# Optimization experiments

Hardware: AMD Instinct MI355X
Metric: run time of the kernel (lower is better)

Reference implementation:

```python
import jax, jax.numpy as jnp
import numpy as np

N_CHANNELS = 270
N_SUBJECTS = 200
B, T = 256, 1024


def setup_inputs() -> dict:
    key = jax.random.key(0)
    k_x, k_s = jax.random.split(key)
    x = jax.random.normal(k_x, (B, N_CHANNELS, T), dtype=jnp.float32)
    subjects = jax.random.randint(k_s, (B,), 0, N_SUBJECTS, dtype=jnp.int64)
    # init_id=True: weights start as identity, then divided by sqrt(C)
    weights = jnp.broadcast_to(jnp.eye(N_CHANNELS, dtype=jnp.float32),
                               (N_SUBJECTS, N_CHANNELS, N_CHANNELS)) / np.sqrt(N_CHANNELS)
    return {"x": x, "subjects": subjects, "weights": weights}


def reference(x, subjects, weights):
    # Gather per-sample CxC weight, then batched matmul: bct,bcd->bdt
    w = weights[subjects]  # (B, C, C)
    return jnp.einsum('bct,bcd->bdt', x, w)
```

## Files before the change

kernel.cpp:

```cpp
#include <hip/hip_runtime.h>


#define C_    270
#define T_    1024
#define B_    256
#define NSUB_ 200

#define BM 64
#define BN 128
#define BK 32
#define NK 9
#define ROWU32 20
#define BOFF (BM * ROWU32)
#define LDSU32 ((BM + BN) * ROWU32)

typedef __attribute__((ext_vector_type(8))) short bf16x8;
typedef __attribute__((ext_vector_type(4))) float f32x4;
typedef __attribute__((ext_vector_type(2))) float f32x2;
typedef __attribute__((ext_vector_type(2))) unsigned u32x2;
typedef __attribute__((ext_vector_type(4))) int i32x4;

__device__ __forceinline__ unsigned pk(float lo, float hi) {
    unsigned r;
    asm("v_cvt_pk_bf16_f32 %0, %1, %2" : "=v"(r) : "v"(lo), "v"(hi));
    return r;
}

__device__ __forceinline__ void tile_barrier() {
    asm volatile("s_waitcnt lgkmcnt(0)" ::: "memory");
    __builtin_amdgcn_s_barrier();
}

template<bool SW>
__device__ __forceinline__ bf16x8 ldfrag(const unsigned* p) {
    i32x4 u = *(const i32x4*)p;
    if (SW) { i32x4 v = {u[2], u[3], u[0], u[1]}; return __builtin_bit_cast(bf16x8, v); }
    return __builtin_bit_cast(bf16x8, u);
}

__global__ __launch_bounds__(256, 3)
void subj_layers_kernel(const float* __restrict__ x,
                        const int* __restrict__ subjects,
                        const float* __restrict__ w,
                        float* __restrict__ out)
{
    __shared__ unsigned lds[2][LDSU32];

    const int tid  = threadIdx.x;
    const int lane = tid & 63;
    const int wid  = tid >> 6;
    const int wr   = wid >> 1;
    const int wc   = wid & 1;
    const int lg   = lane >> 4;
    const int lr   = lane & 15;

    const int bid  = (blockIdx.x & 7) * 1280 + (blockIdx.x >> 3);
    const int b    = bid / 40;
    const int rem  = bid % 40;
    const int d0   = (rem % 5) * BM;
    const int t0   = (rem / 5) * BN;

    int sub = subjects[b];
    sub = sub < 0 ? 0 : (sub >= NSUB_ ? NSUB_ - 1 : sub);
    const float* __restrict__ wsub = w + (size_t)sub * (C_ * C_);
    const float* __restrict__ xb   = x + (size_t)b * (C_ * T_);

    const int btq = tid & 31;
    const int bcq = tid >> 5;
    const float* __restrict__ xbt = xb + (t0 + 4 * btq);
    const int colB = 2 * (bcq ^ ((btq >> 2) & 7));
    const int adp = tid & 31;
    const int acq = tid >> 5;
    const int dA  = d0 + 2 * adp;
    const bool dAok = (dA + 1 < C_);
    const int colA = 2 * (acq ^ ((adp >> 3) & 7));

    f32x4 acc[2][4];
    #pragma unroll
    for (int m = 0; m < 2; ++m)
        #pragma unroll
        for (int n = 0; n < 4; ++n)
            acc[m][n] = (f32x4){0.f, 0.f, 0.f, 0.f};

    f32x4 pb[4];
    f32x2 pa[4];

    auto load_tiles = [&](int c0, bool full) {
        #pragma unroll
        for (int e = 0; e < 4; ++e) {
            const int c = c0 + 4 * bcq + e;
            pb[e] = (full || c < C_) ? *(const f32x4*)(xbt + (size_t)c * T_)
                                     : (f32x4){0.f, 0.f, 0.f, 0.f};
        }
        #pragma unroll
        for (int e = 0; e < 4; ++e) {
            const int c = c0 + 4 * acq + e;
            pa[e] = (dAok && (full || c < C_)) ? *(const f32x2*)(wsub + (size_t)c * C_ + dA)
                                               : (f32x2){0.f, 0.f};
        }
    };

    auto store_tiles = [&](unsigned* L) {
        unsigned* LB = L + BOFF;
        #pragma unroll
        for (int j = 0; j < 4; ++j) {
            const int r = 4 * btq + j;
            u32x2 v;
            v.x = pk(pb[0][j], pb[1][j]);
            v.y = pk(pb[2][j], pb[3][j]);
            *(u32x2*)(LB + r * ROWU32 + colB) = v;
        }
        #pragma unroll
        for (int j = 0; j < 2; ++j) {
            const int r = 2 * adp + j;
            u32x2 v;
            v.x = pk(pa[0][j], pa[1][j]);
            v.y = pk(pa[2][j], pa[3][j]);
            *(u32x2*)(L + r * ROWU32 + colA) = v;
        }
    };

    auto compute = [&](const unsigned* L) {
        const unsigned* LB = L + BOFF;
        bf16x8 af[2], bfr[4];
        const int ab = wr * 32;
        af[0] = ldfrag<false>(L + (ab +  0 + lr) * ROWU32 + 4 * (lg ^ wr));
        af[1] = ldfrag<true >(L + (ab + 16 + lr) * ROWU32 + 4 * (lg ^ wr));
        const int bb = wc * 64;
        bfr[0] = ldfrag<false>(LB + (bb +  0 + lr) * ROWU32 + 4 * (lg ^ (((bb +  0) >> 5) & 3)));
        bfr[1] = ldfrag<true >(LB + (bb + 16 + lr) * ROWU32 + 4 * (lg ^ (((bb + 16) >> 5) & 3)));
        bfr[2] = ldfrag<false>(LB + (bb + 32 + lr) * ROWU32 + 4 * (lg ^ (((bb + 32) >> 5) & 3)));
        bfr[3] = ldfrag<true >(LB + (bb + 48 + lr) * ROWU32 + 4 * (lg ^ (((bb + 48) >> 5) & 3)));
        #pragma unroll
        for (int m = 0; m < 2; ++m)
            #pragma unroll
            for (int n = 0; n < 4; ++n)
                acc[m][n] = __builtin_amdgcn_mfma_f32_16x16x32_bf16(af[m], bfr[n], acc[m][n], 0, 0, 0);
    };

    load_tiles(0, true);
    store_tiles(&lds[0][0]);
    load_tiles(BK, true);
    tile_barrier();

    #pragma unroll 1
    for (int k = 0; k < 6; ++k) {
        compute(&lds[k & 1][0]);
        store_tiles(&lds[(k + 1) & 1][0]);
        load_tiles((k + 2) * BK, true);
        tile_barrier();
    }
    compute(&lds[0][0]);
    store_tiles(&lds[1][0]);
    load_tiles(8 * BK, false);
    tile_barrier();
    compute(&lds[1][0]);
    store_tiles(&lds[0][0]);
    tile_barrier();
    compute(&lds[0][0]);

    float* outb = out + (size_t)b * (C_ * T_);
    #pragma unroll
    for (int m = 0; m < 2; ++m) {
        const int dbase = d0 + wr * 32 + m * 16 + 4 * lg;
        #pragma unroll
        for (int n = 0; n < 4; ++n) {
            const int t = t0 + wc * 64 + n * 16 + lr;
            #pragma unroll
            for (int rr = 0; rr < 4; ++rr) {
                const int d = dbase + rr;
                if (d < C_)
                    outb[(size_t)d * T_ + t] = acc[m][n][rr];
            }
        }
    }
}

extern "C" void kernel_launch(void* const* d_in, const int* in_sizes, int n_in,
                              void* d_out, int out_size, void* d_ws, size_t ws_size,
                              hipStream_t stream)
{
    const float* x        = (const float*)d_in[0];
    const int*   subjects = (const int*)d_in[1];
    const float* w        = (const float*)d_in[2];
    float* out            = (float*)d_out;

    dim3 grid(B_ * 40);
    dim3 block(256);
    hipLaunchKernelGGL(subj_layers_kernel, grid, block, 0, stream,
                       x, subjects, w, out);
}
```

Measured before the change: 203.7 us.

## Stage fp32 tiles via global_load_lds and convert to bf16 at fragment load

Replaces the register-staged load, convert and LDS store path with direct global-to-LDS async loads (global_load_lds) of fp32 tiles. The bf16 conversion moves into the compute step, where each fragment is built from scalar fp32 LDS reads. This removes the register round trip and store instructions and lets loads overlap compute. In exchange it doubles the LDS footprint, uses many scalar LDS reads with possible bank conflicts, and handles the tail by clamping addresses and zeroing fragments.

```diff
diff --git a/kernel.cpp b/kernel.cpp
--- a/kernel.cpp
+++ b/kernel.cpp
@@ -9,15 +9,12 @@
 #define BM 64
 #define BN 128
 #define BK 32
-#define NK 9
-#define ROWU32 20
-#define BOFF (BM * ROWU32)
-#define LDSU32 ((BM + BN) * ROWU32)
+#define LB_U32 (BK * BN)
+#define LA_U32 (BK * BM)
+#define BUF_U32 (LB_U32 + LA_U32)
 
 typedef __attribute__((ext_vector_type(8))) short bf16x8;
 typedef __attribute__((ext_vector_type(4))) float f32x4;
-typedef __attribute__((ext_vector_type(2))) float f32x2;
-typedef __attribute__((ext_vector_type(2))) unsigned u32x2;
 typedef __attribute__((ext_vector_type(4))) int i32x4;
 
 __device__ __forceinline__ unsigned pk(float lo, float hi) {
@@ -26,16 +23,15 @@
     return r;
 }
 
-__device__ __forceinline__ void tile_barrier() {
-    asm volatile("s_waitcnt lgkmcnt(0)" ::: "memory");
-    __builtin_amdgcn_s_barrier();
+__device__ __forceinline__ void gl2lds16(const float* g, const unsigned* l) {
+    __builtin_amdgcn_global_load_lds(
+        (__attribute__((address_space(1))) void*)g,
+        (__attribute__((address_space(3))) void*)l, 16, 0, 0);
 }
-
-template<bool SW>
-__device__ __forceinline__ bf16x8 ldfrag(const unsigned* p) {
-    i32x4 u = *(const i32x4*)p;
-    if (SW) { i32x4 v = {u[2], u[3], u[0], u[1]}; return __builtin_bit_cast(bf16x8, v); }
-    return __builtin_bit_cast(bf16x8, u);
+__device__ __forceinline__ void gl2lds4(const float* g, const unsigned* l) {
+    __builtin_amdgcn_global_load_lds(
+        (__attribute__((address_space(1))) void*)g,
+        (__attribute__((address_space(3))) void*)l, 4, 0, 0);
 }
 
 __global__ __launch_bounds__(256, 3)
@@ -44,7 +40,7 @@
                         const float* __restrict__ w,
                         float* __restrict__ out)
 {
-    __shared__ unsigned lds[2][LDSU32];
+    __shared__ unsigned lds[2][BUF_U32];
 
     const int tid  = threadIdx.x;
     const int lane = tid & 63;
@@ -53,6 +49,7 @@
     const int wc   = wid & 1;
     const int lg   = lane >> 4;
     const int lr   = lane & 15;
+    const int l5   = lane >> 5, l31 = lane & 31;
 
     const int bid  = (blockIdx.x & 7) * 1280 + (blockIdx.x >> 3);
     const int b    = bid / 40;
@@ -64,16 +61,40 @@
     sub = sub < 0 ? 0 : (sub >= NSUB_ ? NSUB_ - 1 : sub);
     const float* __restrict__ wsub = w + (size_t)sub * (C_ * C_);
     const float* __restrict__ xb   = x + (size_t)b * (C_ * T_);
+    const float* wLast = w + (size_t)NSUB_ * C_ * C_ - 1;
 
-    const int btq = tid & 31;
-    const int bcq = tid >> 5;
-    const float* __restrict__ xbt = xb + (t0 + 4 * btq);
-    const int colB = 2 * (bcq ^ ((btq >> 2) & 7));
-    const int adp = tid & 31;
-    const int acq = tid >> 5;
-    const int dA  = d0 + 2 * adp;
-    const bool dAok = (dA + 1 < C_);
-    const int colA = 2 * (acq ^ ((adp >> 3) & 7));
+    const float* xg = xb + (size_t)l5 * T_ + t0 + 4 * l31;
+    const float* ag = wsub + d0 + lane;
+
+    auto stage_full = [&](unsigned* L, int c0) {
+        #pragma unroll
+        for (int ii = 0; ii < 4; ++ii) {
+            const int i = wid + 4 * ii;
+            gl2lds16(xg + (size_t)(c0 + 2 * i) * T_, L + i * 256);
+        }
+        #pragma unroll
+        for (int ii = 0; ii < 8; ++ii) {
+            const int i = wid + 4 * ii;
+            gl2lds4(ag + (size_t)(c0 + i) * C_, L + LB_U32 + i * 64);
+        }
+    };
+
+    auto stage_tail = [&](unsigned* L) {
+        #pragma unroll
+        for (int ii = 0; ii < 4; ++ii) {
+            const int i = wid + 4 * ii;
+            int c = 256 + 2 * i + l5; c = c < C_ ? c : C_ - 1;
+            gl2lds16(xb + (size_t)c * T_ + t0 + 4 * l31, L + i * 256);
+        }
+        #pragma unroll
+        for (int ii = 0; ii < 8; ++ii) {
+            const int i = wid + 4 * ii;
+            int c = 256 + i; c = c < C_ ? c : C_ - 1;
+            const float* ga = ag + (size_t)c * C_;
+            if (ga > wLast) ga = wLast;
+            gl2lds4(ga, L + LB_U32 + i * 64);
+        }
+    };
 
     f32x4 acc[2][4];
     #pragma unroll
@@ -82,55 +103,33 @@
         for (int n = 0; n < 4; ++n)
             acc[m][n] = (f32x4){0.f, 0.f, 0.f, 0.f};
 
-    f32x4 pb[4];
-    f32x2 pa[4];
-
-    auto load_tiles = [&](int c0, bool full) {
+    auto compute = [&](const unsigned* L, bool tail) {
+        const float* Bt = (const float*)L;
+        const float* At = (const float*)(L + LB_U32);
+        const int crel = 2 * lg;
+        bf16x8 af[2], bfr[4];
         #pragma unroll
-        for (int e = 0; e < 4; ++e) {
-            const int c = c0 + 4 * bcq + e;
-            pb[e] = (full || c < C_) ? *(const f32x4*)(xbt + (size_t)c * T_)
-                                     : (f32x4){0.f, 0.f, 0.f, 0.f};
+        for (int m = 0; m < 2; ++m) {
+            const float* p = At + (size_t)crel * BM + (wr * 32 + m * 16 + lr);
+            i32x4 u;
+            #pragma unroll
+            for (int j = 0; j < 4; ++j)
+                u[j] = (int)pk(p[j * 8 * BM], p[j * 8 * BM + BM]);
+            af[m] = __builtin_bit_cast(bf16x8, u);
         }
         #pragma unroll
-        for (int e = 0; e < 4; ++e) {
-            const int c = c0 + 4 * acq + e;
-            pa[e] = (dAok && (full || c < C_)) ? *(const f32x2*)(wsub + (size_t)c * C_ + dA)
-                                               : (f32x2){0.f, 0.f};
+        for (int n = 0; n < 4; ++n) {
+            const float* p = Bt + (size_t)crel * BN + (wc * 64 + n * 16 + lr);
+            i32x4 u;
+            #pragma unroll
+            for (int j = 0; j < 4; ++j)
+                u[j] = (int)pk(p[j * 8 * BN], p[j * 8 * BN + BN]);
+            if (tail) {
+                u[2] = 0; u[3] = 0;
+                if (lg == 3) u[1] = 0;
+            }
+            bfr[n] = __builtin_bit_cast(bf16x8, u);
         }
-    };
-
-    auto store_tiles = [&](unsigned* L) {
-        unsigned* LB = L + BOFF;
-        #pragma unroll
-        for (int j = 0; j < 4; ++j) {
-            const int r = 4 * btq + j;
-            u32x2 v;
-            v.x = pk(pb[0][j], pb[1][j]);
-            v.y = pk(pb[2][j], pb[3][j]);
-            *(u32x2*)(LB + r * ROWU32 + colB) = v;
-        }
-        #pragma unroll
-        for (int j = 0; j < 2; ++j) {
-            const int r = 2 * adp + j;
-            u32x2 v;
-            v.x = pk(pa[0][j], pa[1][j]);
-            v.y = pk(pa[2][j], pa[3][j]);
-            *(u32x2*)(L + r * ROWU32 + colA) = v;
-        }
-    };
-
-    auto compute = [&](const unsigned* L) {
-        const unsigned* LB = L + BOFF;
-        bf16x8 af[2], bfr[4];
-        const int ab = wr * 32;
-        af[0] = ldfrag<false>(L + (ab +  0 + lr) * ROWU32 + 4 * (lg ^ wr));
-        af[1] = ldfrag<true >(L + (ab + 16 + lr) * ROWU32 + 4 * (lg ^ wr));
-        const int bb = wc * 64;
-        bfr[0] = ldfrag<false>(LB + (bb +  0 + lr) * ROWU32 + 4 * (lg ^ (((bb +  0) >> 5) & 3)));
-        bfr[1] = ldfrag<true >(LB + (bb + 16 + lr) * ROWU32 + 4 * (lg ^ (((bb + 16) >> 5) & 3)));
-        bfr[2] = ldfrag<false>(LB + (bb + 32 + lr) * ROWU32 + 4 * (lg ^ (((bb + 32) >> 5) & 3)));
-        bfr[3] = ldfrag<true >(LB + (bb + 48 + lr) * ROWU32 + 4 * (lg ^ (((bb + 48) >> 5) & 3)));
         #pragma unroll
         for (int m = 0; m < 2; ++m)
             #pragma unroll
@@ -138,26 +137,19 @@
                 acc[m][n] = __builtin_amdgcn_mfma_f32_16x16x32_bf16(af[m], bfr[n], acc[m][n], 0, 0, 0);
     };
 
-    load_tiles(0, true);
-    store_tiles(&lds[0][0]);
-    load_tiles(BK, true);
-    tile_barrier();
+    stage_full(&lds[0][0], 0);
+    __syncthreads();
 
     #pragma unroll 1
-    for (int k = 0; k < 6; ++k) {
-        compute(&lds[k & 1][0]);
-        store_tiles(&lds[(k + 1) & 1][0]);
-        load_tiles((k + 2) * BK, true);
-        tile_barrier();
+    for (int k = 0; k < 7; ++k) {
+        stage_full(&lds[(k + 1) & 1][0], (k + 1) * BK);
+        compute(&lds[k & 1][0], false);
+        __syncthreads();
     }
-    compute(&lds[0][0]);
-    store_tiles(&lds[1][0]);
-    load_tiles(8 * BK, false);
-    tile_barrier();
-    compute(&lds[1][0]);
-    store_tiles(&lds[0][0]);
-    tile_barrier();
-    compute(&lds[0][0]);
+    stage_tail(&lds[0][0]);
+    compute(&lds[1][0], false);
+    __syncthreads();
+    compute(&lds[0][0], true);
 
     float* outb = out + (size_t)b * (C_ * T_);
     #pragma unroll
```

New measurement: 203.9 us. About the same (+0.1%).
